# Optimization experiments

Hardware: AMD Instinct MI355X
Metric: run time of the kernel (lower is better)

## Reference

```python
import jax, jax.numpy as jnp
import numpy as np

WS = 8          # window size -> N = 64
SHIFT = 4       # shift size for shifted windows
FEAT = 32       # feature map H = W at stage 3
C = 512         # channels (SwinV2-B stage 3)
HEADS = 16
B_IMG = 128     # images -> 128 * (32/8)^2 = 2048 windows


def _rel_coords_table():
    # log-spaced continuous relative coords table, SwinV2 style: [(2W-1)^2, 2]
    r = np.arange(-(WS - 1), WS, dtype=np.float32)
    t = np.stack(np.meshgrid(r, r, indexing='ij'), axis=-1)  # [15,15,2]
    t = t / (WS - 1) * 8.0
    t = np.sign(t) * np.log2(np.abs(t) + 1.0) / np.log2(8.0)
    return t.reshape(-1, 2)


def _rel_pos_index():
    c = np.stack(np.meshgrid(np.arange(WS), np.arange(WS), indexing='ij'))  # [2,8,8]
    cf = c.reshape(2, -1)
    rel = (cf[:, :, None] - cf[:, None, :]).transpose(1, 2, 0)  # [64,64,2]
    rel[:, :, 0] += WS - 1
    rel[:, :, 1] += WS - 1
    rel[:, :, 0] *= 2 * WS - 1
    return rel.sum(-1).astype(np.int32)  # [64,64]


def _shift_mask():
    # standard SwinV2 shifted-window attention mask: [nW, N, N] in {0, -100}
    img = np.zeros((FEAT, FEAT), dtype=np.float32)
    cnt = 0
    for hs in (slice(0, -WS), slice(-WS, -SHIFT), slice(-SHIFT, None)):
        for ws in (slice(0, -WS), slice(-WS, -SHIFT), slice(-SHIFT, None)):
            img[hs, ws] = cnt
            cnt += 1
    win = img.reshape(FEAT // WS, WS, FEAT // WS, WS).transpose(0, 2, 1, 3)
    win = win.reshape(-1, WS * WS)  # [nW, 64]
    diff = win[:, None, :] - win[:, :, None]
    return np.where(diff != 0, -100.0, 0.0).astype(np.float32)


def setup_inputs() -> dict:
    key = jax.random.key(0)
    ks = jax.random.split(key, 10)
    nW = (FEAT // WS) ** 2  # 16 windows per image
    Bw = B_IMG * nW         # 2048
    N = WS * WS
    s = 0.02
    return {
        'x': jax.random.normal(ks[0], (Bw, N, C), jnp.float32),
        'mask': jnp.asarray(_shift_mask()),
        'qkv_w': jax.random.normal(ks[1], (3 * C, C), jnp.float32) * s,
        'q_bias': jnp.zeros((C,), jnp.float32),
        'v_bias': jnp.zeros((C,), jnp.float32),
        'logit_scale': jnp.full((HEADS, 1, 1), np.log(10.0), jnp.float32),
        'cpb_w1': jax.random.normal(ks[2], (512, 2), jnp.float32) * s,
        'cpb_b1': jnp.zeros((512,), jnp.float32),
        'cpb_w2': jax.random.normal(ks[3], (HEADS, 512), jnp.float32) * s,
        'proj_w': jax.random.normal(ks[4], (C, C), jnp.float32) * s,
        'proj_b': jnp.zeros((C,), jnp.float32),
        'rel_coords_table': jnp.asarray(_rel_coords_table()),
        'rel_pos_index': jnp.asarray(_rel_pos_index()),
    }


def reference(x, mask, qkv_w, q_bias, v_bias, logit_scale, cpb_w1, cpb_b1,
              cpb_w2, proj_w, proj_b, rel_coords_table, rel_pos_index):
    Bw, N, Cdim = x.shape
    H = logit_scale.shape[0]
    d = Cdim // H
    # qkv projection; k has no bias (SwinV2)
    qkv_bias = jnp.concatenate([q_bias, jnp.zeros_like(q_bias), v_bias])
    qkv = (x @ qkv_w.T + qkv_bias).reshape(Bw, N, 3, H, d).transpose(2, 0, 3, 1, 4)
    q, k, v = qkv[0], qkv[1], qkv[2]  # each [Bw,H,N,d]
    # cosine attention with learned per-head temperature
    qn = q / jnp.maximum(jnp.linalg.norm(q, axis=-1, keepdims=True), 1e-12)
    kn = k / jnp.maximum(jnp.linalg.norm(k, axis=-1, keepdims=True), 1e-12)
    attn = jnp.einsum('bhnd,bhmd->bhnm', qn, kn)
    scale = jnp.exp(jnp.minimum(logit_scale, jnp.log(100.0)))  # [H,1,1]
    attn = attn * scale[None]
    # continuous relative position bias via small MLP over log-spaced coords
    tbl = jax.nn.relu(rel_coords_table @ cpb_w1.T + cpb_b1) @ cpb_w2.T  # [(2W-1)^2,H]
    bias = tbl[rel_pos_index.reshape(-1)].reshape(N, N, H).transpose(2, 0, 1)
    attn = attn + 16.0 * jax.nn.sigmoid(bias)[None]
    # shifted-window mask applied per window group
    nW = mask.shape[0]
    attn = attn.reshape(Bw // nW, nW, H, N, N) + mask[None, :, None]
    attn = jax.nn.softmax(attn.reshape(Bw, H, N, N), axis=-1)
    out = jnp.einsum('bhnm,bhmd->bhnd', attn, v)
    out = out.transpose(0, 2, 1, 3).reshape(Bw, N, Cdim)
    return out @ proj_w.T + proj_b
```

## Files before the change

### kernel.cpp

```cpp
#include <hip/hip_runtime.h>
#include <stdint.h>
#include <stddef.h>


typedef __attribute__((ext_vector_type(8))) short bf16x8;
typedef __attribute__((ext_vector_type(4))) float f32x4;
typedef __attribute__((ext_vector_type(4))) unsigned short us4;
typedef __attribute__((ext_vector_type(8))) unsigned short us8;
typedef unsigned short u16;
typedef unsigned int u32;

#define FENCE() asm volatile("" ::: "memory")
#define WAITV4() asm volatile("s_waitcnt vmcnt(4)" ::: "memory")
#define WAITV0() asm volatile("s_waitcnt vmcnt(0)" ::: "memory")
#define WAITL0() asm volatile("s_waitcnt lgkmcnt(0)" ::: "memory")

__device__ __forceinline__ u16 f2bf(float f) {
  union { __bf16 b; u16 u; } cv;
  cv.b = (__bf16)f;
  return cv.u;
}
__device__ __forceinline__ float bf2f(u16 s) {
  return __uint_as_float(((u32)s) << 16);
}
__device__ __forceinline__ void gl_lds16(const void* g, void* l) {
  __builtin_amdgcn_global_load_lds(
      (const __attribute__((address_space(1))) u32*)g,
      (__attribute__((address_space(3))) u32*)l, 16, 0, 0);
}
__device__ __forceinline__ f32x4 mfma16(bf16x8 a, bf16x8 b, f32x4 c) {
  return __builtin_amdgcn_mfma_f32_16x16x32_bf16(a, b, c, 0, 0, 0);
}
__device__ __forceinline__ bf16x8 ldswz(const u16* p, int ks) {
  return *(const bf16x8*)((const u16*)((uintptr_t)p ^ (uintptr_t)(ks << 6)));
}


__global__ void conv_w_kernel(const float* __restrict__ QW, const float* __restrict__ PW,
                              u16* __restrict__ WQB, u16* __restrict__ WPB) {
  int idx = blockIdx.x * 256 + threadIdx.x;
  const int NQ = 1536 * 512 / 4;
  float4 v; u16* dst;
  if (idx < NQ) { v = ((const float4*)QW)[idx]; dst = WQB + (size_t)idx * 4; }
  else { int k = idx - NQ; v = ((const float4*)PW)[k]; dst = WPB + (size_t)k * 4; }
  us4 u; u.x = f2bf(v.x); u.y = f2bf(v.y); u.z = f2bf(v.z); u.w = f2bf(v.w);
  *(us4*)dst = u;
}

__global__ void xconv_kernel(const float* __restrict__ X, u16* __restrict__ XB) {
  size_t idx = (size_t)blockIdx.x * 256 + threadIdx.x;
  float4 a = ((const float4*)X)[idx * 2];
  float4 b = ((const float4*)X)[idx * 2 + 1];
  us8 o;
  o[0] = f2bf(a.x); o[1] = f2bf(a.y); o[2] = f2bf(a.z); o[3] = f2bf(a.w);
  o[4] = f2bf(b.x); o[5] = f2bf(b.y); o[6] = f2bf(b.z); o[7] = f2bf(b.w);
  *(us8*)&XB[idx * 8] = o;
}

__global__ void sig16_kernel(const float* __restrict__ CT, const float* __restrict__ W1,
                             const float* __restrict__ B1, const float* __restrict__ W2,
                             float* __restrict__ SIG) {
  int i = blockIdx.x;
  int tid = threadIdx.x;
  float c0 = CT[i * 2 + 0], c1 = CT[i * 2 + 1];
  float a[16];
  #pragma unroll
  for (int hh = 0; hh < 16; ++hh) a[hh] = 0.f;
  #pragma unroll
  for (int jj = 0; jj < 2; ++jj) {
    int j = tid + jj * 256;
    float h = fmaxf(c0 * W1[j * 2 + 0] + c1 * W1[j * 2 + 1] + B1[j], 0.f);
    #pragma unroll
    for (int hh = 0; hh < 16; ++hh) a[hh] += h * W2[hh * 512 + j];
  }
  __shared__ float red[4][16];
  #pragma unroll
  for (int hh = 0; hh < 16; ++hh) {
    float v = a[hh];
    for (int m = 1; m < 64; m <<= 1) v += __shfl_xor(v, m);
    if ((tid & 63) == 0) red[tid >> 6][hh] = v;
  }
  __syncthreads();
  if (tid < 16) {
    float v = red[0][tid] + red[1][tid] + red[2][tid] + red[3][tid];
    SIG[i * 16 + tid] = 16.f / (1.f + __expf(-v));
  }
}

__global__ void cmb_kernel(const float* __restrict__ SIG, const float* __restrict__ MASK,
                           const int* __restrict__ RPI, float* __restrict__ CMB) {
  int b = blockIdx.x;
  int w = b >> 4, h = b & 15;
  int tid = threadIdx.x;
  const float* mrow = &MASK[(size_t)w * 4096];
  float* crow = &CMB[(size_t)b * 4096];
  #pragma unroll
  for (int it = 0; it < 16; ++it) {
    int nm = it * 256 + tid;
    crow[nm] = SIG[RPI[nm] * 16 + h] + mrow[nm];
  }
}


#define MFMA_QUAD(MB, NB, B0, B1)                                          \
  FENCE(); __builtin_amdgcn_s_barrier(); FENCE();                          \
  WAITL0(); __builtin_amdgcn_sched_barrier(0);                             \
  __builtin_amdgcn_s_setprio(1);                                           \
  _Pragma("unroll")                                                        \
  for (int m = 0; m < 4; ++m)                                              \
    _Pragma("unroll")                                                      \
    for (int n = 0; n < 2; ++n) {                                          \
      acc[(MB) + m][(NB) + n] = mfma16(af0[m], B0[n], acc[(MB) + m][(NB) + n]); \
      acc[(MB) + m][(NB) + n] = mfma16(af1[m], B1[n], acc[(MB) + m][(NB) + n]); \
    }                                                                      \
  __builtin_amdgcn_s_setprio(0);                                           \
  FENCE(); __builtin_amdgcn_s_barrier(); FENCE();

#define GEMM8_KLOOP()                                                      \
  for (int t = 0; t < 8; ++t) {                                            \
    const int buf = (t & 1) * 32768;                                       \
                                                                   \
    _Pragma("unroll")                                                      \
    for (int m = 0; m < 4; ++m) {                                          \
      const u16* pA = &S[buf + (wm * 64 + m * 16 + fr) * 64 + fsw];        \
      af0[m] = ldswz(pA, 0); af1[m] = ldswz(pA, 1);                        \
    }                                                                      \
    _Pragma("unroll")                                                      \
    for (int n = 0; n < 2; ++n) {                                          \
      const u16* pB = &S[buf + 16384 + (wn * 32 + n * 16 + fr) * 64 + fsw];\
      b00[n] = ldswz(pB, 0); b01[n] = ldswz(pB, 1);                        \
    }                                                                      \
    if (t < 7) stageB(t + 1, 1);                                           \
    MFMA_QUAD(0, 0, b00, b01)                                              \
                                                                   \
    _Pragma("unroll")                                                      \
    for (int n = 0; n < 2; ++n) {                                          \
      const u16* pB = &S[buf + 16384 + (128 + wn * 32 + n * 16 + fr) * 64 + fsw]; \
      b10[n] = ldswz(pB, 0); b11[n] = ldswz(pB, 1);                        \
    }                                                                      \
    if (t < 7) stageA(t + 1, 1);                                           \
    MFMA_QUAD(0, 2, b10, b11)                                              \
                                                                   \
    _Pragma("unroll")                                                      \
    for (int m = 0; m < 4; ++m) {                                          \
      const u16* pA = &S[buf + (128 + wm * 64 + m * 16 + fr) * 64 + fsw];  \
      af0[m] = ldswz(pA, 0); af1[m] = ldswz(pA, 1);                        \
    }                                                                      \
    if (t < 6) stageA(t + 2, 0);                                           \
    MFMA_QUAD(4, 2, b10, b11)                                              \
                                                                   \
    if (t < 6) { stageB(t + 2, 0); WAITV4(); }                             \
    else if (t == 6) { WAITV0(); }                                         \
    MFMA_QUAD(4, 0, b00, b01)                                              \
  }


__global__ __launch_bounds__(512, 1) void qkv_gemm8(
    const u16* __restrict__ XB, const u16* __restrict__ WB,
    const float* __restrict__ QB, const float* __restrict__ VB,
    u16* __restrict__ QKV) {
  __shared__ u16 S[65536];
  const int tid = threadIdx.x, lane = tid & 63, w = tid >> 6;
  int bid = blockIdx.x;
  int swz = (bid & 7) * 384 + (bid >> 3);
  const int mt = swz / 6, nt = swz - mt * 6;
  const long m0 = (long)mt * 256, n0 = (long)nt * 256;
  const int wm = w >> 2, wn = w & 3;
  const int fr = lane & 15, lg = lane >> 4;
  const int fsw = (lg ^ (lane & 7)) << 3;
  const f32x4 zf = {0.f, 0.f, 0.f, 0.f};

  f32x4 acc[8][4];
  #pragma unroll
  for (int mi = 0; mi < 8; ++mi)
    #pragma unroll
    for (int ni = 0; ni < 4; ++ni) acc[mi][ni] = zf;

  auto stageA = [&](int kt, int h) {
    int dst = (kt & 1) * 32768 + h * 8192;
    #pragma unroll
    for (int i = 0; i < 2; ++i) {
      int ch = i * 512 + tid;
      int row = ch >> 3, kcs = (ch & 7) ^ (row & 7);
      gl_lds16(&XB[(size_t)(m0 + h * 128 + row) * 512 + kt * 64 + kcs * 8],
               &S[dst + (i * 512 + w * 64) * 8]);
    }
  };
  auto stageB = [&](int kt, int h) {
    int dst = (kt & 1) * 32768 + 16384 + h * 8192;
    #pragma unroll
    for (int i = 0; i < 2; ++i) {
      int ch = i * 512 + tid;
      int row = ch >> 3, kcs = (ch & 7) ^ (row & 7);
      gl_lds16(&WB[(size_t)(n0 + h * 128 + row) * 512 + kt * 64 + kcs * 8],
               &S[dst + (i * 512 + w * 64) * 8]);
    }
  };

  bf16x8 af0[4], af1[4], b00[2], b01[2], b10[2], b11[2];

  stageA(0, 0); stageB(0, 0); stageB(0, 1); stageA(0, 1);
  stageA(1, 0); stageB(1, 0);
  WAITV4();
  FENCE(); __builtin_amdgcn_s_barrier(); FENCE();

  GEMM8_KLOOP()

  #pragma unroll
  for (int ni = 0; ni < 4; ++ni) {
    const long c = n0 + (ni >> 1) * 128 + wn * 32 + (ni & 1) * 16 + fr;
    float bias = (c < 512) ? QB[c] : (c < 1024 ? 0.f : VB[c - 1024]);
    #pragma unroll
    for (int mi = 0; mi < 8; ++mi)
      #pragma unroll
      for (int r = 0; r < 4; ++r) {
        long row = m0 + (mi >> 2) * 128 + wm * 64 + (mi & 3) * 16 + lg * 4 + r;
        QKV[row * 1536 + c] = f2bf(acc[mi][ni][r] + bias);
      }
  }
}


__global__ __launch_bounds__(512, 1) void proj_gemm8(
    const u16* __restrict__ A, const u16* __restrict__ WB,
    const float* __restrict__ PB, float* __restrict__ OUT) {
  __shared__ u16 S[65536];
  const int tid = threadIdx.x, lane = tid & 63, w = tid >> 6;
  int bid = blockIdx.x;
  int swz = (bid & 7) * 128 + (bid >> 3);
  const int mt = swz >> 1, nt = swz & 1;
  const long m0 = (long)mt * 256, n0 = (long)nt * 256;
  const int wm = w >> 2, wn = w & 3;
  const int fr = lane & 15, lg = lane >> 4;
  const int fsw = (lg ^ (lane & 7)) << 3;
  const f32x4 zf = {0.f, 0.f, 0.f, 0.f};

  f32x4 acc[8][4];
  #pragma unroll
  for (int mi = 0; mi < 8; ++mi)
    #pragma unroll
    for (int ni = 0; ni < 4; ++ni) acc[mi][ni] = zf;

  auto stageA = [&](int kt, int h) {
    int dst = (kt & 1) * 32768 + h * 8192;
    #pragma unroll
    for (int i = 0; i < 2; ++i) {
      int ch = i * 512 + tid;
      int row = ch >> 3, kcs = (ch & 7) ^ (row & 7);
      gl_lds16(&A[(size_t)(m0 + h * 128 + row) * 1536 + kt * 64 + kcs * 8],
               &S[dst + (i * 512 + w * 64) * 8]);
    }
  };
  auto stageB = [&](int kt, int h) {
    int dst = (kt & 1) * 32768 + 16384 + h * 8192;
    #pragma unroll
    for (int i = 0; i < 2; ++i) {
      int ch = i * 512 + tid;
      int row = ch >> 3, kcs = (ch & 7) ^ (row & 7);
      gl_lds16(&WB[(size_t)(n0 + h * 128 + row) * 512 + kt * 64 + kcs * 8],
               &S[dst + (i * 512 + w * 64) * 8]);
    }
  };

  bf16x8 af0[4], af1[4], b00[2], b01[2], b10[2], b11[2];

  stageA(0, 0); stageB(0, 0); stageB(0, 1); stageA(0, 1);
  stageA(1, 0); stageB(1, 0);
  WAITV4();
  FENCE(); __builtin_amdgcn_s_barrier(); FENCE();

  GEMM8_KLOOP()

  #pragma unroll
  for (int ni = 0; ni < 4; ++ni) {
    const long c = n0 + (ni >> 1) * 128 + wn * 32 + (ni & 1) * 16 + fr;
    float bias = PB[c];
    #pragma unroll
    for (int mi = 0; mi < 8; ++mi)
      #pragma unroll
      for (int r = 0; r < 4; ++r) {
        long row = m0 + (mi >> 2) * 128 + wm * 64 + (mi & 3) * 16 + lg * 4 + r;
        OUT[row * 512 + c] = acc[mi][ni][r] + bias;
      }
  }
}


__global__ __launch_bounds__(256, 2) void qkv_gemm_rs(
    const float* __restrict__ X, const u16* __restrict__ WB,
    const float* __restrict__ QB, const float* __restrict__ VB,
    u16* __restrict__ QKV) {
  __shared__ u16 As[128 * 64];
  __shared__ u16 Bs[128 * 64];
  const int tid = threadIdx.x, lane = tid & 63, w = tid >> 6;
  int bid = blockIdx.x;
  int swz = (bid & 7) * 1536 + (bid >> 3);
  const int mt = swz / 12, nt = swz - mt * 12;
  const long m0 = (long)mt * 128, n0 = (long)nt * 128;
  const int wm = w >> 1, wn = w & 1;
  const f32x4 zf = {0.f, 0.f, 0.f, 0.f};

  f32x4 acc[4][4];
  #pragma unroll
  for (int mi = 0; mi < 4; ++mi)
    #pragma unroll
    for (int ni = 0; ni < 4; ++ni) acc[mi][ni] = zf;

  const int fr = lane & 15;
  const int fsw = ((lane >> 4) ^ (lane & 7)) * 8;
  const u16* Ap = &As[(wm * 64 + fr) * 64 + fsw];
  const u16* Bp = &Bs[(wn * 64 + fr) * 64 + fsw];

  for (int t = 0; t < 8; ++t) {
    float4 av[8];
    #pragma unroll
    for (int i = 0; i < 8; ++i) {
      int ch = tid + (i << 8);
      int row = ch >> 4, kc = ch & 15;
      av[i] = *(const float4*)&X[(m0 + row) * 512 + t * 64 + kc * 4];
    }
    #pragma unroll
    for (int i = 0; i < 4; ++i) {
      int ch = ((w << 2) + i) * 64 + lane;
      int row = ch >> 3, kc = (ch & 7) ^ (row & 7);
      gl_lds16(&WB[(n0 + row) * 512 + t * 64 + kc * 8], &Bs[((w << 2) + i) * 512]);
    }
    #pragma unroll
    for (int i = 0; i < 8; ++i) {
      int ch = tid + (i << 8);
      int row = ch >> 4, kc = ch & 15;
      int kcs = kc ^ ((row & 7) << 1);
      us4 u; u.x = f2bf(av[i].x); u.y = f2bf(av[i].y); u.z = f2bf(av[i].z); u.w = f2bf(av[i].w);
      *(us4*)&As[row * 64 + kcs * 4] = u;
    }
    __syncthreads();
    #pragma unroll
    for (int ks = 0; ks < 2; ++ks) {
      bf16x8 af[4], bfr[4];
      #pragma unroll
      for (int mi = 0; mi < 4; ++mi) af[mi] = ldswz(Ap + mi * 1024, ks);
      #pragma unroll
      for (int ni = 0; ni < 4; ++ni) bfr[ni] = ldswz(Bp + ni * 1024, ks);
      #pragma unroll
      for (int mi = 0; mi < 4; ++mi)
        #pragma unroll
        for (int ni = 0; ni < 4; ++ni)
          acc[mi][ni] = mfma16(af[mi], bfr[ni], acc[mi][ni]);
    }
    __syncthreads();
  }

  #pragma unroll
  for (int ni = 0; ni < 4; ++ni) {
    const long c = n0 + wn * 64 + ni * 16 + (lane & 15);
    float bias = (c < 512) ? QB[c] : (c < 1024 ? 0.f : VB[c - 1024]);
    #pragma unroll
    for (int mi = 0; mi < 4; ++mi)
      #pragma unroll
      for (int r = 0; r < 4; ++r) {
        long row = m0 + wm * 64 + mi * 16 + (lane >> 4) * 4 + r;
        QKV[row * 1536 + c] = f2bf(acc[mi][ni][r] + bias);
      }
  }
}


__global__ __launch_bounds__(256, 4) void attn_kernel(
    u16* __restrict__ QKV, const float* __restrict__ CMB, const float* __restrict__ LS) {
  __shared__ u16 sm[7424];
  u16* qs = sm;
  u16* ksm = sm + 2560;
  u16* ps = sm;
  u16* vt = sm + 5120;
  const int tid = threadIdx.x, lane = tid & 63, w = tid >> 6;
  const int b = blockIdx.x, wi = b & 15;
  const size_t base = (size_t)b * 64 * 1536;
  const int cl = lane & 15, lg = lane >> 4;
  const int srow = tid >> 2, sck = tid & 3;
  const int vd = tid & 31, vkb = tid >> 5;
  const f32x4 zf = {0.f, 0.f, 0.f, 0.f};

  for (int h = 0; h < 16; ++h) {
    const float scale = __expf(fminf(LS[h], 4.6051702f));
    {
      us8 qv = *(const us8*)&QKV[base + (size_t)srow * 1536 + h * 32 + sck * 8];
      float qf[8]; float ss = 0.f;
      #pragma unroll
      for (int j = 0; j < 8; ++j) { qf[j] = bf2f(qv[j]); ss += qf[j] * qf[j]; }
      ss += __shfl_xor(ss, 1); ss += __shfl_xor(ss, 2);
      float rn = scale / fmaxf(sqrtf(ss), 1e-12f);
      us8 qo;
      #pragma unroll
      for (int j = 0; j < 8; ++j) qo[j] = f2bf(qf[j] * rn);
      *(us8*)&qs[srow * 40 + sck * 8] = qo;
    }
    {
      us8 kv = *(const us8*)&QKV[base + (size_t)srow * 1536 + 512 + h * 32 + sck * 8];
      float kf[8]; float ss = 0.f;
      #pragma unroll
      for (int j = 0; j < 8; ++j) { kf[j] = bf2f(kv[j]); ss += kf[j] * kf[j]; }
      ss += __shfl_xor(ss, 1); ss += __shfl_xor(ss, 2);
      float rn = 1.f / fmaxf(sqrtf(ss), 1e-12f);
      us8 ko;
      #pragma unroll
      for (int j = 0; j < 8; ++j) ko[j] = f2bf(kf[j] * rn);
      *(us8*)&ksm[srow * 40 + sck * 8] = ko;
    }
    {
      us8 vo;
      #pragma unroll
      for (int e = 0; e < 8; ++e)
        vo[e] = QKV[base + (size_t)(vkb * 8 + e) * 1536 + 1024 + h * 32 + vd];
      *(us8*)&vt[vd * 72 + vkb * 8] = vo;
    }
    __syncthreads();

    bf16x8 aq = *(const bf16x8*)&qs[(w * 16 + cl) * 40 + lg * 8];
    f32x4 s4[4];
    #pragma unroll
    for (int nt = 0; nt < 4; ++nt) {
      bf16x8 bk = *(const bf16x8*)&ksm[(nt * 16 + cl) * 40 + lg * 8];
      s4[nt] = mfma16(aq, bk, zf);
    }

    const float* cp = &CMB[((size_t)(wi * 16 + h)) << 12];
    const int r0 = w * 16 + lg * 4;
    float p[4][4];
    #pragma unroll
    for (int r = 0; r < 4; ++r) {
      float mx = -3.0e38f;
      #pragma unroll
      for (int q4 = 0; q4 < 4; ++q4) {
        float v = s4[q4][r] + cp[(r0 + r) * 64 + q4 * 16 + cl];
        p[q4][r] = v; mx = fmaxf(mx, v);
      }
      mx = fmaxf(mx, __shfl_xor(mx, 1));
      mx = fmaxf(mx, __shfl_xor(mx, 2));
      mx = fmaxf(mx, __shfl_xor(mx, 4));
      mx = fmaxf(mx, __shfl_xor(mx, 8));
      float sum = 0.f;
      #pragma unroll
      for (int q4 = 0; q4 < 4; ++q4) { float e = __expf(p[q4][r] - mx); p[q4][r] = e; sum += e; }
      sum += __shfl_xor(sum, 1); sum += __shfl_xor(sum, 2);
      sum += __shfl_xor(sum, 4); sum += __shfl_xor(sum, 8);
      float inv = 1.f / sum;
      #pragma unroll
      for (int q4 = 0; q4 < 4; ++q4) p[q4][r] *= inv;
    }
    __syncthreads();

    #pragma unroll
    for (int r = 0; r < 4; ++r)
      #pragma unroll
      for (int q4 = 0; q4 < 4; ++q4)
        ps[(r0 + r) * 72 + q4 * 16 + cl] = f2bf(p[q4][r]);

    f32x4 o4[2]; o4[0] = zf; o4[1] = zf;
    #pragma unroll
    for (int ks = 0; ks < 2; ++ks) {
      bf16x8 ap = *(const bf16x8*)&ps[(w * 16 + cl) * 72 + ks * 32 + lg * 8];
      #pragma unroll
      for (int n2 = 0; n2 < 2; ++n2) {
        bf16x8 bv = *(const bf16x8*)&vt[(n2 * 16 + cl) * 72 + ks * 32 + lg * 8];
        o4[n2] = mfma16(ap, bv, o4[n2]);
      }
    }
    #pragma unroll
    for (int n2 = 0; n2 < 2; ++n2)
      #pragma unroll
      for (int r = 0; r < 4; ++r)
        QKV[base + (size_t)(w * 16 + lg * 4 + r) * 1536 + h * 32 + n2 * 16 + cl] = f2bf(o4[n2][r]);
    __syncthreads();
  }
}


extern "C" void kernel_launch(void* const* d_in, const int* in_sizes, int n_in,
                              void* d_out, int out_size, void* d_ws, size_t ws_size,
                              hipStream_t stream) {
  const float* X    = (const float*)d_in[0];
  const float* MASK = (const float*)d_in[1];
  const float* QW   = (const float*)d_in[2];
  const float* QB   = (const float*)d_in[3];
  const float* VB   = (const float*)d_in[4];
  const float* LS   = (const float*)d_in[5];
  const float* CW1  = (const float*)d_in[6];
  const float* CB1  = (const float*)d_in[7];
  const float* CW2  = (const float*)d_in[8];
  const float* PW   = (const float*)d_in[9];
  const float* PB   = (const float*)d_in[10];
  const float* CT   = (const float*)d_in[11];
  const int*   RPI  = (const int*)d_in[12];
  float* OUT = (float*)d_out;

  char* ws = (char*)d_ws;
  const bool big = ws_size >= 543178752ull;
  u16* QKV = (u16*)ws;
  u16* XB  = (u16*)(ws + 402653184ull);
  size_t off = big ? 536870912ull : 402653184ull;
  float* CMB = (float*)(ws + off);  off += 4194304ull;
  float* SIG = (float*)(ws + off);  off += 16384ull;
  u16*   WQB = (u16*)(ws + off);    off += 1572864ull;
  u16*   WPB = (u16*)(ws + off);

  conv_w_kernel<<<1024, 256, 0, stream>>>(QW, PW, WQB, WPB);
  sig16_kernel<<<225, 256, 0, stream>>>(CT, CW1, CB1, CW2, SIG);
  cmb_kernel<<<256, 256, 0, stream>>>(SIG, MASK, RPI, CMB);
  if (big) {
    xconv_kernel<<<32768, 256, 0, stream>>>(X, XB);
    qkv_gemm8<<<3072, 512, 0, stream>>>(XB, WQB, QB, VB, QKV);
  } else {
    qkv_gemm_rs<<<12288, 256, 0, stream>>>(X, WQB, QB, VB, QKV);
  }
  attn_kernel<<<2048, 256, 0, stream>>>(QKV, CMB, LS);
  proj_gemm8<<<1024, 512, 0, stream>>>(QKV, WPB, PB, OUT);
}
```

Before: 777.4 us.

## Replace 256x256 proj GEMM with simpler 128x128 tile, 2 blocks/CU

The output projection GEMM now uses 128x128 tiles with 256 threads and two blocks per CU, instead of a 256x256 tile with 512 threads and a double-buffered, barrier-interleaved pipeline. The new version uses a single-buffered LDS stage with syncthreads around each k-step. It trades global-load/MFMA overlap inside a block for more blocks in flight and a simpler schedule. The shared MFMA_QUAD macro is also reordered so all af0 MFMAs issue before the af1 ones, which removes back-to-back dependent accumulations.

```diff
diff --git a/kernel.cpp b/kernel.cpp
--- a/kernel.cpp
+++ b/kernel.cpp
@@ -109,10 +109,13 @@
   _Pragma("unroll")                                                        \
   for (int m = 0; m < 4; ++m)                                              \
     _Pragma("unroll")                                                      \
-    for (int n = 0; n < 2; ++n) {                                          \
+    for (int n = 0; n < 2; ++n)                                            \
       acc[(MB) + m][(NB) + n] = mfma16(af0[m], B0[n], acc[(MB) + m][(NB) + n]); \
+  _Pragma("unroll")                                                        \
+  for (int m = 0; m < 4; ++m)                                              \
+    _Pragma("unroll")                                                      \
+    for (int n = 0; n < 2; ++n)                                            \
       acc[(MB) + m][(NB) + n] = mfma16(af1[m], B1[n], acc[(MB) + m][(NB) + n]); \
-    }                                                                      \
   __builtin_amdgcn_s_setprio(0);                                           \
   FENCE(); __builtin_amdgcn_s_barrier(); FENCE();
 
@@ -221,65 +224,64 @@
 }
 
 
-__global__ __launch_bounds__(512, 1) void proj_gemm8(
+__global__ __launch_bounds__(256, 2) void proj_gemm(
     const u16* __restrict__ A, const u16* __restrict__ WB,
     const float* __restrict__ PB, float* __restrict__ OUT) {
-  __shared__ u16 S[65536];
+  __shared__ u16 As[128 * 64];
+  __shared__ u16 Bs[128 * 64];
   const int tid = threadIdx.x, lane = tid & 63, w = tid >> 6;
   int bid = blockIdx.x;
-  int swz = (bid & 7) * 128 + (bid >> 3);
-  const int mt = swz >> 1, nt = swz & 1;
-  const long m0 = (long)mt * 256, n0 = (long)nt * 256;
-  const int wm = w >> 2, wn = w & 3;
-  const int fr = lane & 15, lg = lane >> 4;
-  const int fsw = (lg ^ (lane & 7)) << 3;
+  int swz = (bid & 7) * 512 + (bid >> 3);
+  const int mt = swz >> 2, nt = swz & 3;
+  const long m0 = (long)mt * 128, n0 = (long)nt * 128;
+  const int wm = w >> 1, wn = w & 1;
   const f32x4 zf = {0.f, 0.f, 0.f, 0.f};
 
-  f32x4 acc[8][4];
-  #pragma unroll
-  for (int mi = 0; mi < 8; ++mi)
+  f32x4 acc[4][4];
+  #pragma unroll
+  for (int mi = 0; mi < 4; ++mi)
     #pragma unroll
     for (int ni = 0; ni < 4; ++ni) acc[mi][ni] = zf;
 
-  auto stageA = [&](int kt, int h) {
-    int dst = (kt & 1) * 32768 + h * 8192;
-    #pragma unroll
-    for (int i = 0; i < 2; ++i) {
-      int ch = i * 512 + tid;
-      int row = ch >> 3, kcs = (ch & 7) ^ (row & 7);
-      gl_lds16(&A[(size_t)(m0 + h * 128 + row) * 1536 + kt * 64 + kcs * 8],
-               &S[dst + (i * 512 + w * 64) * 8]);
-    }
-  };
-  auto stageB = [&](int kt, int h) {
-    int dst = (kt & 1) * 32768 + 16384 + h * 8192;
-    #pragma unroll
-    for (int i = 0; i < 2; ++i) {
-      int ch = i * 512 + tid;
-      int row = ch >> 3, kcs = (ch & 7) ^ (row & 7);
-      gl_lds16(&WB[(size_t)(n0 + h * 128 + row) * 512 + kt * 64 + kcs * 8],
-               &S[dst + (i * 512 + w * 64) * 8]);
-    }
-  };
-
-  bf16x8 af0[4], af1[4], b00[2], b01[2], b10[2], b11[2];
-
-  stageA(0, 0); stageB(0, 0); stageB(0, 1); stageA(0, 1);
-  stageA(1, 0); stageB(1, 0);
-  WAITV4();
-  FENCE(); __builtin_amdgcn_s_barrier(); FENCE();
-
-  GEMM8_KLOOP()
+  const int fr = lane & 15;
+  const int fsw = ((lane >> 4) ^ (lane & 7)) * 8;
+  const u16* Ap = &As[(wm * 64 + fr) * 64 + fsw];
+  const u16* Bp = &Bs[(wn * 64 + fr) * 64 + fsw];
+
+  for (int t = 0; t < 8; ++t) {
+    #pragma unroll
+    for (int i = 0; i < 4; ++i) {
+      int ch = ((w << 2) + i) * 64 + lane;
+      int row = ch >> 3, kc = (ch & 7) ^ (row & 7);
+      gl_lds16(&A[(m0 + row) * 1536 + t * 64 + kc * 8], &As[((w << 2) + i) * 512]);
+      gl_lds16(&WB[(n0 + row) * 512 + t * 64 + kc * 8], &Bs[((w << 2) + i) * 512]);
+    }
+    __syncthreads();
+    #pragma unroll
+    for (int ks = 0; ks < 2; ++ks) {
+      bf16x8 af[4], bfr[4];
+      #pragma unroll
+      for (int mi = 0; mi < 4; ++mi) af[mi] = ldswz(Ap + mi * 1024, ks);
+      #pragma unroll
+      for (int ni = 0; ni < 4; ++ni) bfr[ni] = ldswz(Bp + ni * 1024, ks);
+      #pragma unroll
+      for (int mi = 0; mi < 4; ++mi)
+        #pragma unroll
+        for (int ni = 0; ni < 4; ++ni)
+          acc[mi][ni] = mfma16(af[mi], bfr[ni], acc[mi][ni]);
+    }
+    __syncthreads();
+  }
 
   #pragma unroll
   for (int ni = 0; ni < 4; ++ni) {
-    const long c = n0 + (ni >> 1) * 128 + wn * 32 + (ni & 1) * 16 + fr;
+    const long c = n0 + wn * 64 + ni * 16 + fr;
     float bias = PB[c];
     #pragma unroll
-    for (int mi = 0; mi < 8; ++mi)
+    for (int mi = 0; mi < 4; ++mi)
       #pragma unroll
       for (int r = 0; r < 4; ++r) {
-        long row = m0 + (mi >> 2) * 128 + wm * 64 + (mi & 3) * 16 + lg * 4 + r;
+        long row = m0 + wm * 64 + mi * 16 + (lane >> 4) * 4 + r;
         OUT[row * 512 + c] = acc[mi][ni][r] + bias;
       }
   }
@@ -513,5 +515,5 @@
     qkv_gemm_rs<<<12288, 256, 0, stream>>>(X, WQB, QB, VB, QKV);
   }
   attn_kernel<<<2048, 256, 0, stream>>>(QKV, CMB, LS);
-  proj_gemm8<<<1024, 512, 0, stream>>>(QKV, WPB, PB, OUT);
-}
+  proj_gemm<<<4096, 256, 0, stream>>>(QKV, WPB, PB, OUT);
+}
```

Measured after the change: 760.6 us. 2.2% less time.
